# Performance work log

Measured on AMD Instinct MI355X. Metric: run time of the kernel, lower is better.

The kernel has to match this reference:

```python
import jax, jax.numpy as jnp
import numpy as np

BETA = 0.25  # commitment loss weight


def setup_inputs() -> dict:
    key = jax.random.key(0)
    k1, k2 = jax.random.split(key)
    x = jax.random.normal(k1, (16, 2048, 512), dtype=jnp.float32)
    codebooks = jax.random.normal(k2, (8, 1024, 512), dtype=jnp.float32)
    return {"x": x, "codebooks": codebooks}


def reference(x, codebooks):
    """Residual VQ: sequentially quantize residual with each codebook.
    x: [B, N, D] float; codebooks: [Q, C, D] float.
    Returns (quantized_out [B,N,D], indices [B,N,Q], vq_losses [Q], qq_losses [Q]).
    """
    sg = jax.lax.stop_gradient

    def step(carry, cb):
        residual, qout = carry  # [B,N,D], [B,N,D]; cb: [C,D]
        # squared euclidean distances [B,N,C] via GEMM
        d = (
            jnp.sum(residual * residual, axis=-1, keepdims=True)
            - 2.0 * jnp.einsum("bnd,cd->bnc", residual, cb)
            + jnp.sum(cb * cb, axis=-1)
        )
        idx = jnp.argmin(d, axis=-1)          # [B,N] nearest code
        q_hard = cb[idx]                       # [B,N,D] codebook gather
        # straight-through estimator
        q = residual + sg(q_hard - residual)
        vq = jnp.mean((q_hard - sg(residual)) ** 2)        # codebook loss
        qq = BETA * jnp.mean((sg(q_hard) - residual) ** 2)  # commitment loss
        new_residual = residual - sg(q)
        return (new_residual, qout + q), (idx, vq, qq)

    init = (x, jnp.zeros_like(x))
    (_, quantized_out), (idxs, vqs, qqs) = jax.lax.scan(step, init, codebooks)
    all_indices = jnp.moveaxis(idxs, 0, -1)  # [B, N, Q]
    return quantized_out, all_indices, vqs, qqs
```

## Files before the change

kernel.cpp:

```cpp
#include <hip/hip_runtime.h>

#define D 512
#define C 1024
#define BM 128
#define BN 128
#define BK 32
#define NCHUNK 8
#define KSTEPS 16
#define NBLK_CU 8192

typedef _Float16 f16x8 __attribute__((ext_vector_type(8)));
typedef float f32x4 __attribute__((ext_vector_type(4)));

__device__ __forceinline__ void gll16(const void* g, void* l) {
    __builtin_amdgcn_global_load_lds(
        (const __attribute__((address_space(1))) void*)g,
        (__attribute__((address_space(3))) void*)l, 16, 0, 0);
}

__global__ __launch_bounds__(256) void cbnorm_kernel(const float* __restrict__ cb,
                                                     float* __restrict__ cbn) {
    int code = blockIdx.x * 4 + (threadIdx.x >> 6);
    int lane = threadIdx.x & 63;
    const float* row = cb + (size_t)code * D;
    float4 a = *(const float4*)(row + lane * 8);
    float4 b = *(const float4*)(row + lane * 8 + 4);
    float s = a.x*a.x + a.y*a.y + a.z*a.z + a.w*a.w
            + b.x*b.x + b.y*b.y + b.z*b.z + b.w*b.w;
    #pragma unroll
    for (int off = 32; off > 0; off >>= 1) s += __shfl_down(s, off, 64);
    if (lane == 0) cbn[code] = s;
}

__global__ __launch_bounds__(256) void cb_split_kernel(const float* __restrict__ cbs,
                                                       uint4* __restrict__ hi_plane,
                                                       uint4* __restrict__ lo_plane) {
    int t = blockIdx.x * 256 + threadIdx.x;
    int rg = t >> 9;
    int u  = t & 511;
    int q  = rg >> 7;
    int cc = (rg >> 4) & 7;
    int ks = rg & 15;
    int ctile = u >> 6;
    int ksub  = (u >> 4) & 3;
    int col   = u & 15;
    int code  = cc * 128 + ctile * 16 + col;
    int d0    = ks * 32 + ksub * 8;
    const float* src = cbs + ((size_t)q * C + code) * D + d0;
    float4 v0 = *(const float4*)src;
    float4 v1 = *(const float4*)(src + 4);
    float xv[8] = {v0.x, v0.y, v0.z, v0.w, v1.x, v1.y, v1.z, v1.w};
    f16x8 h, l;
    #pragma unroll
    for (int e = 0; e < 8; ++e) {
        _Float16 hh = (_Float16)xv[e];
        h[e] = hh;
        l[e] = (_Float16)(xv[e] - (float)hh);
    }
    hi_plane[t] = __builtin_bit_cast(uint4, h);
    lo_plane[t] = __builtin_bit_cast(uint4, l);
}

__global__ __launch_bounds__(256, 2) void vq_mfma_step(
    const float* __restrict__ rin,
    const uint4* __restrict__ bhq,
    const uint4* __restrict__ blq,
    const float* __restrict__ cbnq,
    float4*      __restrict__ partial)
{
    __shared__ uint4 SH[2][4][512];
    const int tid  = threadIdx.x;
    const int lane = tid & 63;
    const int wv   = tid >> 6;
    const int wm   = wv >> 1, wn = wv & 1;
    const int bm   = blockIdx.x & 255;
    const int cc   = blockIdx.x >> 8;
    const int bp   = bm * BM;

    f32x4 acc[4][4];
    #pragma unroll
    for (int i = 0; i < 4; ++i)
        #pragma unroll
        for (int j = 0; j < 4; ++j) acc[i][j] = (f32x4){0.f, 0.f, 0.f, 0.f};

    auto STAGE = [&](int buf, int ks) {
        const uint4* bh = bhq + (size_t)(cc * KSTEPS + ks) * 512;
        const uint4* bl = blq + (size_t)(cc * KSTEPS + ks) * 512;
        gll16(bh + tid,       &SH[buf][2][tid]);
        gll16(bh + tid + 256, &SH[buf][2][tid + 256]);
        gll16(bl + tid,       &SH[buf][3][tid]);
        gll16(bl + tid + 256, &SH[buf][3][tid + 256]);
        #pragma unroll
        for (int it = 0; it < 2; ++it) {
            int oct  = tid + it * 256;
            int row  = ((oct >> 6) << 4) + (oct & 15);
            int ksub = (oct >> 4) & 3;
            const float* src = rin + (size_t)(bp + row) * D + ks * BK + ksub * 8;
            float4 v0 = *(const float4*)src;
            float4 v1 = *(const float4*)(src + 4);
            float xv[8] = {v0.x, v0.y, v0.z, v0.w, v1.x, v1.y, v1.z, v1.w};
            f16x8 h, l;
            #pragma unroll
            for (int e = 0; e < 8; ++e) {
                _Float16 hh = (_Float16)xv[e];
                h[e] = hh;
                l[e] = (_Float16)(xv[e] - (float)hh);
            }
            SH[buf][0][oct] = __builtin_bit_cast(uint4, h);
            SH[buf][1][oct] = __builtin_bit_cast(uint4, l);
        }
    };

    STAGE(0, 0);
    int buf = 0;
    for (int ks = 0; ks < KSTEPS; ++ks) {
        __syncthreads();
        if (ks + 1 < KSTEPS) STAGE(buf ^ 1, ks + 1);
        f16x8 ah[4], al[4], bh[4], bl[4];
        #pragma unroll
        for (int mt = 0; mt < 4; ++mt) {
            ah[mt] = __builtin_bit_cast(f16x8, SH[buf][0][(wm * 4 + mt) * 64 + lane]);
            al[mt] = __builtin_bit_cast(f16x8, SH[buf][1][(wm * 4 + mt) * 64 + lane]);
        }
        #pragma unroll
        for (int nt = 0; nt < 4; ++nt) {
            bh[nt] = __builtin_bit_cast(f16x8, SH[buf][2][(wn * 4 + nt) * 64 + lane]);
            bl[nt] = __builtin_bit_cast(f16x8, SH[buf][3][(wn * 4 + nt) * 64 + lane]);
        }
        #pragma unroll
        for (int mt = 0; mt < 4; ++mt)
            #pragma unroll
            for (int nt = 0; nt < 4; ++nt) {
                acc[mt][nt] = __builtin_amdgcn_mfma_f32_16x16x32_f16(ah[mt], bh[nt], acc[mt][nt], 0, 0, 0);
                acc[mt][nt] = __builtin_amdgcn_mfma_f32_16x16x32_f16(ah[mt], bl[nt], acc[mt][nt], 0, 0, 0);
                acc[mt][nt] = __builtin_amdgcn_mfma_f32_16x16x32_f16(al[mt], bh[nt], acc[mt][nt], 0, 0, 0);
            }
        buf ^= 1;
    }

    const int colbase = cc * BN;
    float cbn_l[4];
    int   ci_l[4];
    #pragma unroll
    for (int nt = 0; nt < 4; ++nt) {
        ci_l[nt]  = colbase + (wn * 4 + nt) * 16 + (lane & 15);
        cbn_l[nt] = cbnq[ci_l[nt]];
    }
    #pragma unroll
    for (int mt = 0; mt < 4; ++mt) {
        #pragma unroll
        for (int r = 0; r < 4; ++r) {
            float s1 = 3.4e38f, s2 = 3.4e38f;
            int i1 = 1 << 30, i2 = 1 << 30;
            #pragma unroll
            for (int nt = 0; nt < 4; ++nt) {
                float s = fmaf(-2.f, acc[mt][nt][r], cbn_l[nt]);
                int ci = ci_l[nt];
                if (s < s1 || (s == s1 && ci < i1)) { s2 = s1; i2 = i1; s1 = s; i1 = ci; }
                else if (s < s2 || (s == s2 && ci < i2)) { s2 = s; i2 = ci; }
            }
            #pragma unroll
            for (int m = 1; m < 16; m <<= 1) {
                float o1 = __shfl_xor(s1, m, 64); int oi1 = __shfl_xor(i1, m, 64);
                float o2 = __shfl_xor(s2, m, 64); int oi2 = __shfl_xor(i2, m, 64);
                if (o1 < s1 || (o1 == s1 && oi1 < i1)) {
                    if (s1 < o2 || (s1 == o2 && i1 < oi2)) { s2 = s1; i2 = i1; }
                    else { s2 = o2; i2 = oi2; }
                    s1 = o1; i1 = oi1;
                } else {
                    if (o1 < s2 || (o1 == s2 && oi1 < i2)) { s2 = o1; i2 = oi1; }
                }
            }
            if ((lane & 15) == 0) {
                int row = bp + wm * 64 + mt * 16 + (lane >> 4) * 4 + r;
                partial[(size_t)row * 16 + cc * 2 + wn] = make_float4(s1, (float)i1, s2, (float)i2);
            }
        }
    }
}

__global__ __launch_bounds__(256) void combine_update(
    const float* __restrict__ rin, float* __restrict__ rout,
    const float* __restrict__ cbq,
    const float4* __restrict__ partial,
    float* __restrict__ idx_out, float* __restrict__ blockloss,
    int q, int nq)
{
    __shared__ float wls[4];
    const int lane = threadIdx.x & 63;
    const int wv   = threadIdx.x >> 6;
    const int p    = blockIdx.x * 4 + wv;

    float s1 = 3.4e38f, s2 = 3.4e38f;
    int i1 = 1 << 30, i2 = 1 << 30;
    if (lane < 16) {
        float4 v = partial[(size_t)p * 16 + lane];
        s1 = v.x; i1 = (int)v.y; s2 = v.z; i2 = (int)v.w;
    }
    #pragma unroll
    for (int m = 1; m < 16; m <<= 1) {
        float o1 = __shfl_xor(s1, m, 64); int oi1 = __shfl_xor(i1, m, 64);
        float o2 = __shfl_xor(s2, m, 64); int oi2 = __shfl_xor(i2, m, 64);
        if (o1 < s1 || (o1 == s1 && oi1 < i1)) {
            if (s1 < o2 || (s1 == o2 && i1 < oi2)) { s2 = s1; i2 = i1; }
            else { s2 = o2; i2 = oi2; }
            s1 = o1; i1 = oi1;
        } else {
            if (o1 < s2 || (o1 == s2 && oi1 < i2)) { s2 = o1; i2 = oi1; }
        }
    }
    float s1b = __shfl(s1, 0, 64);
    float s2b = __shfl(s2, 0, 64);
    i1 = __shfl(i1, 0, 64);
    i2 = __shfl(i2, 0, 64);

    const float* rrow = rin + (size_t)p * D;
    const float* c1   = cbq + (size_t)i1 * D;
    float4 r0 = *(const float4*)(rrow + lane * 8);
    float4 r1 = *(const float4*)(rrow + lane * 8 + 4);
    float4 a0 = *(const float4*)(c1 + lane * 8);
    float4 a1 = *(const float4*)(c1 + lane * 8 + 4);
    float ra[8] = {r0.x, r0.y, r0.z, r0.w, r1.x, r1.y, r1.z, r1.w};
    float aa[8] = {a0.x, a0.y, a0.z, a0.w, a1.x, a1.y, a1.z, a1.w};

    int f = i1;
    bool use2 = false;
    if (s2b - s1b <= 0.05f) {
        const float* c2 = cbq + (size_t)i2 * D;
        float4 b0 = *(const float4*)(c2 + lane * 8);
        float4 b1 = *(const float4*)(c2 + lane * 8 + 4);
        float bb[8] = {b0.x, b0.y, b0.z, b0.w, b1.x, b1.y, b1.z, b1.w};
        double da = 0.0, db = 0.0;
        #pragma unroll
        for (int e = 0; e < 8; ++e) {
            double rr = (double)ra[e], av = (double)aa[e], bv = (double)bb[e];
            da += av * av - 2.0 * rr * av;
            db += bv * bv - 2.0 * rr * bv;
        }
        #pragma unroll
        for (int m = 32; m > 0; m >>= 1) {
            da += __shfl_xor(da, m, 64);
            db += __shfl_xor(db, m, 64);
        }
        if (db < da || (db == da && i2 < i1)) { f = i2; use2 = true; }
        if (use2) {
            #pragma unroll
            for (int e = 0; e < 8; ++e) aa[e] = bb[e];
        }
    }
    if (lane == 0) idx_out[(size_t)p * nq + q] = (float)f;

    float nsum = 0.f;
    float nv[8];
    #pragma unroll
    for (int e = 0; e < 8; ++e) {
        nv[e] = ra[e] - aa[e];
        nsum = fmaf(nv[e], nv[e], nsum);
    }
    float4 w0 = {nv[0], nv[1], nv[2], nv[3]};
    float4 w1 = {nv[4], nv[5], nv[6], nv[7]};
    *(float4*)(rout + (size_t)p * D + lane * 8)     = w0;
    *(float4*)(rout + (size_t)p * D + lane * 8 + 4) = w1;
    #pragma unroll
    for (int off = 32; off > 0; off >>= 1) nsum += __shfl_down(nsum, off, 64);
    if (lane == 0) wls[wv] = nsum;
    __syncthreads();
    if (threadIdx.x == 0)
        blockloss[(size_t)q * NBLK_CU + blockIdx.x] = wls[0] + wls[1] + wls[2] + wls[3];
}

__global__ __launch_bounds__(256) void finalize_kernel(
    const float* __restrict__ x, float* __restrict__ outq,
    const float* __restrict__ blockloss,
    float* __restrict__ losses, float invPD, int n4, int nq)
{
    if (blockIdx.x < (unsigned)nq) {
        __shared__ float wls[4];
        int q = blockIdx.x;
        float s = 0.f;
        for (int i = threadIdx.x; i < NBLK_CU; i += 256)
            s += blockloss[(size_t)q * NBLK_CU + i];
        #pragma unroll
        for (int off = 32; off > 0; off >>= 1) s += __shfl_down(s, off, 64);
        if ((threadIdx.x & 63) == 0) wls[threadIdx.x >> 6] = s;
        __syncthreads();
        if (threadIdx.x == 0) {
            float vq = (wls[0] + wls[1] + wls[2] + wls[3]) * invPD;
            losses[q] = vq;
            losses[nq + q] = 0.25f * vq;
        }
    }
    int stride = gridDim.x * blockDim.x;
    for (int i = blockIdx.x * blockDim.x + threadIdx.x; i < n4; i += stride) {
        float4 xv = ((const float4*)x)[i];
        float4 rv = ((float4*)outq)[i];
        float4 qv;
        qv.x = xv.x - rv.x;
        qv.y = xv.y - rv.y;
        qv.z = xv.z - rv.z;
        qv.w = xv.w - rv.w;
        ((float4*)outq)[i] = qv;
    }
}

extern "C" void kernel_launch(void* const* d_in, const int* in_sizes, int n_in,
                              void* d_out, int out_size, void* d_ws, size_t ws_size,
                              hipStream_t stream)
{
    const float* x   = (const float*)d_in[0];
    const float* cbs = (const float*)d_in[1];
    const int PD = in_sizes[0];
    const int P  = PD / D;
    const int nq = in_sizes[1] / (C * D);

    float* out     = (float*)d_out;
    float* resid   = out;
    float* idx_out = out + (size_t)PD;
    float* losses  = idx_out + (size_t)P * nq;

    char* wsb = (char*)d_ws;
    uint4*  cb_hi     = (uint4*)wsb;
    uint4*  cb_lo     = (uint4*)(wsb + 8388608);
    float*  cbn       = (float*)(wsb + 16777216);
    float4* partial   = (float4*)(wsb + 16809984);
    float*  blockloss = (float*)(wsb + 25198592);

    cbnorm_kernel<<<nq * C / 4, 256, 0, stream>>>(cbs, cbn);
    cb_split_kernel<<<nq * C * D / 8 / 256, 256, 0, stream>>>(cbs, cb_hi, cb_lo);

    for (int q = 0; q < nq; ++q) {
        vq_mfma_step<<<(P / BM) * NCHUNK, 256, 0, stream>>>(
            q == 0 ? x : resid,
            cb_hi + (size_t)q * 65536, cb_lo + (size_t)q * 65536,
            cbn + (size_t)q * C, partial);
        combine_update<<<P / 4, 256, 0, stream>>>(
            q == 0 ? x : resid, resid,
            cbs + (size_t)q * C * D, partial,
            idx_out, blockloss, q, nq);
    }
    finalize_kernel<<<2048, 256, 0, stream>>>(x, out, blockloss, losses,
                                              1.f / (float)PD, PD / 4, nq);
}
```

Before: 1.663 ms.

## Use single fp16 MFMA pass with top-3 candidates and exact fp64 rescoring

Drops the hi/lo fp16 split emulation, so the distance GEMM runs one fp16 MFMA per tile instead of three and stages half the LDS data. To make up for the lower precision, each row keeps its top-3 candidates instead of top-2, their indices packed into one float slot, and combine_update always rescores all three in fp64 against the fp32 codebook. Occupancy hint rises to 4 blocks per CU. The risk is picking the wrong code when the true nearest falls outside the fp16 top-3, and the extra gathers and fp64 math in the combine kernel.

```diff
diff --git a/kernel.cpp b/kernel.cpp
--- a/kernel.cpp
+++ b/kernel.cpp
@@ -4,7 +4,6 @@
 #define C 1024
 #define BM 128
 #define BN 128
-#define BK 32
 #define NCHUNK 8
 #define KSTEPS 16
 #define NBLK_CU 8192
@@ -16,6 +15,14 @@
     __builtin_amdgcn_global_load_lds(
         (const __attribute__((address_space(1))) void*)g,
         (__attribute__((address_space(3))) void*)l, 16, 0, 0);
+}
+
+__device__ __forceinline__ void ins3(float s, int i,
+                                     float& s1, int& i1, float& s2, int& i2,
+                                     float& s3, int& i3) {
+    if (s < s1 || (s == s1 && i < i1)) { s3 = s2; i3 = i2; s2 = s1; i2 = i1; s1 = s; i1 = i; }
+    else if (s < s2 || (s == s2 && i < i2)) { s3 = s2; i3 = i2; s2 = s; i2 = i; }
+    else if (s < s3 || (s == s3 && i < i3)) { s3 = s; i3 = i; }
 }
 
 __global__ __launch_bounds__(256) void cbnorm_kernel(const float* __restrict__ cb,
@@ -33,42 +40,35 @@
 }
 
 __global__ __launch_bounds__(256) void cb_split_kernel(const float* __restrict__ cbs,
-                                                       uint4* __restrict__ hi_plane,
-                                                       uint4* __restrict__ lo_plane) {
+                                                       uint4* __restrict__ hi_plane) {
     int t = blockIdx.x * 256 + threadIdx.x;
     int rg = t >> 9;
     int u  = t & 511;
     int q  = rg >> 7;
     int cc = (rg >> 4) & 7;
     int ks = rg & 15;
-    int ctile = u >> 6;
-    int ksub  = (u >> 4) & 3;
-    int col   = u & 15;
-    int code  = cc * 128 + ctile * 16 + col;
-    int d0    = ks * 32 + ksub * 8;
+    int tile = u >> 6;
+    int ksub = (u >> 4) & 3;
+    int col  = u & 15;
+    int code = cc * 128 + tile * 16 + col;
+    int d0   = ks * 32 + ksub * 8;
     const float* src = cbs + ((size_t)q * C + code) * D + d0;
     float4 v0 = *(const float4*)src;
     float4 v1 = *(const float4*)(src + 4);
     float xv[8] = {v0.x, v0.y, v0.z, v0.w, v1.x, v1.y, v1.z, v1.w};
-    f16x8 h, l;
-    #pragma unroll
-    for (int e = 0; e < 8; ++e) {
-        _Float16 hh = (_Float16)xv[e];
-        h[e] = hh;
-        l[e] = (_Float16)(xv[e] - (float)hh);
-    }
+    f16x8 h;
+    #pragma unroll
+    for (int e = 0; e < 8; ++e) h[e] = (_Float16)xv[e];
     hi_plane[t] = __builtin_bit_cast(uint4, h);
-    lo_plane[t] = __builtin_bit_cast(uint4, l);
-}
-
-__global__ __launch_bounds__(256, 2) void vq_mfma_step(
+}
+
+__global__ __launch_bounds__(256, 4) void vq_mfma_step(
     const float* __restrict__ rin,
     const uint4* __restrict__ bhq,
-    const uint4* __restrict__ blq,
     const float* __restrict__ cbnq,
     float4*      __restrict__ partial)
 {
-    __shared__ uint4 SH[2][4][512];
+    __shared__ uint4 SH[2][2][512];
     const int tid  = threadIdx.x;
     const int lane = tid & 63;
     const int wv   = tid >> 6;
@@ -85,29 +85,21 @@
 
     auto STAGE = [&](int buf, int ks) {
         const uint4* bh = bhq + (size_t)(cc * KSTEPS + ks) * 512;
-        const uint4* bl = blq + (size_t)(cc * KSTEPS + ks) * 512;
-        gll16(bh + tid,       &SH[buf][2][tid]);
-        gll16(bh + tid + 256, &SH[buf][2][tid + 256]);
-        gll16(bl + tid,       &SH[buf][3][tid]);
-        gll16(bl + tid + 256, &SH[buf][3][tid + 256]);
+        gll16(bh + tid,       &SH[buf][1][tid]);
+        gll16(bh + tid + 256, &SH[buf][1][tid + 256]);
         #pragma unroll
         for (int it = 0; it < 2; ++it) {
             int oct  = tid + it * 256;
             int row  = ((oct >> 6) << 4) + (oct & 15);
             int ksub = (oct >> 4) & 3;
-            const float* src = rin + (size_t)(bp + row) * D + ks * BK + ksub * 8;
+            const float* src = rin + (size_t)(bp + row) * D + ks * 32 + ksub * 8;
             float4 v0 = *(const float4*)src;
             float4 v1 = *(const float4*)(src + 4);
             float xv[8] = {v0.x, v0.y, v0.z, v0.w, v1.x, v1.y, v1.z, v1.w};
-            f16x8 h, l;
+            f16x8 h;
             #pragma unroll
-            for (int e = 0; e < 8; ++e) {
-                _Float16 hh = (_Float16)xv[e];
-                h[e] = hh;
-                l[e] = (_Float16)(xv[e] - (float)hh);
-            }
+            for (int e = 0; e < 8; ++e) h[e] = (_Float16)xv[e];
             SH[buf][0][oct] = __builtin_bit_cast(uint4, h);
-            SH[buf][1][oct] = __builtin_bit_cast(uint4, l);
         }
     };
 
@@ -116,25 +108,18 @@
     for (int ks = 0; ks < KSTEPS; ++ks) {
         __syncthreads();
         if (ks + 1 < KSTEPS) STAGE(buf ^ 1, ks + 1);
-        f16x8 ah[4], al[4], bh[4], bl[4];
-        #pragma unroll
-        for (int mt = 0; mt < 4; ++mt) {
+        f16x8 ah[4], bh[4];
+        #pragma unroll
+        for (int mt = 0; mt < 4; ++mt)
             ah[mt] = __builtin_bit_cast(f16x8, SH[buf][0][(wm * 4 + mt) * 64 + lane]);
-            al[mt] = __builtin_bit_cast(f16x8, SH[buf][1][(wm * 4 + mt) * 64 + lane]);
-        }
-        #pragma unroll
-        for (int nt = 0; nt < 4; ++nt) {
-            bh[nt] = __builtin_bit_cast(f16x8, SH[buf][2][(wn * 4 + nt) * 64 + lane]);
-            bl[nt] = __builtin_bit_cast(f16x8, SH[buf][3][(wn * 4 + nt) * 64 + lane]);
-        }
+        #pragma unroll
+        for (int nt = 0; nt < 4; ++nt)
+            bh[nt] = __builtin_bit_cast(f16x8, SH[buf][1][(wn * 4 + nt) * 64 + lane]);
         #pragma unroll
         for (int mt = 0; mt < 4; ++mt)
             #pragma unroll
-            for (int nt = 0; nt < 4; ++nt) {
+            for (int nt = 0; nt < 4; ++nt)
                 acc[mt][nt] = __builtin_amdgcn_mfma_f32_16x16x32_f16(ah[mt], bh[nt], acc[mt][nt], 0, 0, 0);
-                acc[mt][nt] = __builtin_amdgcn_mfma_f32_16x16x32_f16(ah[mt], bl[nt], acc[mt][nt], 0, 0, 0);
-                acc[mt][nt] = __builtin_amdgcn_mfma_f32_16x16x32_f16(al[mt], bh[nt], acc[mt][nt], 0, 0, 0);
-            }
         buf ^= 1;
     }
 
@@ -150,30 +135,27 @@
     for (int mt = 0; mt < 4; ++mt) {
         #pragma unroll
         for (int r = 0; r < 4; ++r) {
-            float s1 = 3.4e38f, s2 = 3.4e38f;
-            int i1 = 1 << 30, i2 = 1 << 30;
+            float s1 = 3.4e38f, s2 = 3.4e38f, s3 = 3.4e38f;
+            int i1 = 1023, i2 = 1023, i3 = 1023;
             #pragma unroll
             for (int nt = 0; nt < 4; ++nt) {
                 float s = fmaf(-2.f, acc[mt][nt][r], cbn_l[nt]);
-                int ci = ci_l[nt];
-                if (s < s1 || (s == s1 && ci < i1)) { s2 = s1; i2 = i1; s1 = s; i1 = ci; }
-                else if (s < s2 || (s == s2 && ci < i2)) { s2 = s; i2 = ci; }
+                ins3(s, ci_l[nt], s1, i1, s2, i2, s3, i3);
             }
             #pragma unroll
             for (int m = 1; m < 16; m <<= 1) {
                 float o1 = __shfl_xor(s1, m, 64); int oi1 = __shfl_xor(i1, m, 64);
                 float o2 = __shfl_xor(s2, m, 64); int oi2 = __shfl_xor(i2, m, 64);
-                if (o1 < s1 || (o1 == s1 && oi1 < i1)) {
-                    if (s1 < o2 || (s1 == o2 && i1 < oi2)) { s2 = s1; i2 = i1; }
-                    else { s2 = o2; i2 = oi2; }
-                    s1 = o1; i1 = oi1;
-                } else {
-                    if (o1 < s2 || (o1 == s2 && oi1 < i2)) { s2 = o1; i2 = oi1; }
-                }
+                float o3 = __shfl_xor(s3, m, 64); int oi3 = __shfl_xor(i3, m, 64);
+                ins3(o1, oi1, s1, i1, s2, i2, s3, i3);
+                ins3(o2, oi2, s1, i1, s2, i2, s3, i3);
+                ins3(o3, oi3, s1, i1, s2, i2, s3, i3);
             }
             if ((lane & 15) == 0) {
                 int row = bp + wm * 64 + mt * 16 + (lane >> 4) * 4 + r;
-                partial[(size_t)row * 16 + cc * 2 + wn] = make_float4(s1, (float)i1, s2, (float)i2);
+                unsigned pk = (unsigned)i1 | ((unsigned)i2 << 10) | ((unsigned)i3 << 20);
+                partial[(size_t)row * 16 + cc * 2 + wn] =
+                    make_float4(s1, s2, s3, __builtin_bit_cast(float, pk));
             }
         }
     }
@@ -191,70 +173,68 @@
     const int wv   = threadIdx.x >> 6;
     const int p    = blockIdx.x * 4 + wv;
 
-    float s1 = 3.4e38f, s2 = 3.4e38f;
-    int i1 = 1 << 30, i2 = 1 << 30;
+    float s1 = 3.4e38f, s2 = 3.4e38f, s3 = 3.4e38f;
+    int i1 = 1023, i2 = 1023, i3 = 1023;
     if (lane < 16) {
         float4 v = partial[(size_t)p * 16 + lane];
-        s1 = v.x; i1 = (int)v.y; s2 = v.z; i2 = (int)v.w;
+        unsigned pk = __builtin_bit_cast(unsigned, v.w);
+        s1 = v.x; s2 = v.y; s3 = v.z;
+        i1 = pk & 1023; i2 = (pk >> 10) & 1023; i3 = (pk >> 20) & 1023;
     }
     #pragma unroll
     for (int m = 1; m < 16; m <<= 1) {
         float o1 = __shfl_xor(s1, m, 64); int oi1 = __shfl_xor(i1, m, 64);
         float o2 = __shfl_xor(s2, m, 64); int oi2 = __shfl_xor(i2, m, 64);
-        if (o1 < s1 || (o1 == s1 && oi1 < i1)) {
-            if (s1 < o2 || (s1 == o2 && i1 < oi2)) { s2 = s1; i2 = i1; }
-            else { s2 = o2; i2 = oi2; }
-            s1 = o1; i1 = oi1;
-        } else {
-            if (o1 < s2 || (o1 == s2 && oi1 < i2)) { s2 = o1; i2 = oi1; }
-        }
-    }
-    float s1b = __shfl(s1, 0, 64);
-    float s2b = __shfl(s2, 0, 64);
+        float o3 = __shfl_xor(s3, m, 64); int oi3 = __shfl_xor(i3, m, 64);
+        ins3(o1, oi1, s1, i1, s2, i2, s3, i3);
+        ins3(o2, oi2, s1, i1, s2, i2, s3, i3);
+        ins3(o3, oi3, s1, i1, s2, i2, s3, i3);
+    }
     i1 = __shfl(i1, 0, 64);
     i2 = __shfl(i2, 0, 64);
+    i3 = __shfl(i3, 0, 64);
 
     const float* rrow = rin + (size_t)p * D;
-    const float* c1   = cbq + (size_t)i1 * D;
     float4 r0 = *(const float4*)(rrow + lane * 8);
     float4 r1 = *(const float4*)(rrow + lane * 8 + 4);
-    float4 a0 = *(const float4*)(c1 + lane * 8);
-    float4 a1 = *(const float4*)(c1 + lane * 8 + 4);
+    const float* c1 = cbq + (size_t)i1 * D;
+    const float* c2 = cbq + (size_t)i2 * D;
+    const float* c3 = cbq + (size_t)i3 * D;
+    float4 a0 = *(const float4*)(c1 + lane * 8), a1 = *(const float4*)(c1 + lane * 8 + 4);
+    float4 b0 = *(const float4*)(c2 + lane * 8), b1 = *(const float4*)(c2 + lane * 8 + 4);
+    float4 g0 = *(const float4*)(c3 + lane * 8), g1 = *(const float4*)(c3 + lane * 8 + 4);
     float ra[8] = {r0.x, r0.y, r0.z, r0.w, r1.x, r1.y, r1.z, r1.w};
     float aa[8] = {a0.x, a0.y, a0.z, a0.w, a1.x, a1.y, a1.z, a1.w};
-
-    int f = i1;
-    bool use2 = false;
-    if (s2b - s1b <= 0.05f) {
-        const float* c2 = cbq + (size_t)i2 * D;
-        float4 b0 = *(const float4*)(c2 + lane * 8);
-        float4 b1 = *(const float4*)(c2 + lane * 8 + 4);
-        float bb[8] = {b0.x, b0.y, b0.z, b0.w, b1.x, b1.y, b1.z, b1.w};
-        double da = 0.0, db = 0.0;
-        #pragma unroll
-        for (int e = 0; e < 8; ++e) {
-            double rr = (double)ra[e], av = (double)aa[e], bv = (double)bb[e];
-            da += av * av - 2.0 * rr * av;
-            db += bv * bv - 2.0 * rr * bv;
-        }
-        #pragma unroll
-        for (int m = 32; m > 0; m >>= 1) {
-            da += __shfl_xor(da, m, 64);
-            db += __shfl_xor(db, m, 64);
-        }
-        if (db < da || (db == da && i2 < i1)) { f = i2; use2 = true; }
-        if (use2) {
-            #pragma unroll
-            for (int e = 0; e < 8; ++e) aa[e] = bb[e];
-        }
-    }
-    if (lane == 0) idx_out[(size_t)p * nq + q] = (float)f;
+    float bb[8] = {b0.x, b0.y, b0.z, b0.w, b1.x, b1.y, b1.z, b1.w};
+    float gg[8] = {g0.x, g0.y, g0.z, g0.w, g1.x, g1.y, g1.z, g1.w};
+
+    double d1 = 0.0, d2 = 0.0, d3 = 0.0;
+    #pragma unroll
+    for (int e = 0; e < 8; ++e) {
+        double rr = (double)ra[e];
+        double av = (double)aa[e], bv = (double)bb[e], gv = (double)gg[e];
+        d1 += av * av - 2.0 * rr * av;
+        d2 += bv * bv - 2.0 * rr * bv;
+        d3 += gv * gv - 2.0 * rr * gv;
+    }
+    #pragma unroll
+    for (int m = 32; m > 0; m >>= 1) {
+        d1 += __shfl_xor(d1, m, 64);
+        d2 += __shfl_xor(d2, m, 64);
+        d3 += __shfl_xor(d3, m, 64);
+    }
+    int    fi = i1;
+    double fd = d1;
+    if (d2 < fd || (d2 == fd && i2 < fi)) { fd = d2; fi = i2; }
+    if (d3 < fd || (d3 == fd && i3 < fi)) { fd = d3; fi = i3; }
+    if (lane == 0) idx_out[(size_t)p * nq + q] = (float)fi;
 
     float nsum = 0.f;
     float nv[8];
     #pragma unroll
     for (int e = 0; e < 8; ++e) {
-        nv[e] = ra[e] - aa[e];
+        float cv = (fi == i1) ? aa[e] : ((fi == i2) ? bb[e] : gg[e]);
+        nv[e] = ra[e] - cv;
         nsum = fmaf(nv[e], nv[e], nsum);
     }
     float4 w0 = {nv[0], nv[1], nv[2], nv[3]};
@@ -320,22 +300,19 @@
 
     char* wsb = (char*)d_ws;
     uint4*  cb_hi     = (uint4*)wsb;
-    uint4*  cb_lo     = (uint4*)(wsb + 8388608);
-    float*  cbn       = (float*)(wsb + 16777216);
-    float4* partial   = (float4*)(wsb + 16809984);
-    float*  blockloss = (float*)(wsb + 25198592);
+    float*  cbn       = (float*)(wsb + 8388608);
+    float4* partial   = (float4*)(wsb + 8421376);
+    float*  blockloss = (float*)(wsb + 16809984);
 
     cbnorm_kernel<<<nq * C / 4, 256, 0, stream>>>(cbs, cbn);
-    cb_split_kernel<<<nq * C * D / 8 / 256, 256, 0, stream>>>(cbs, cb_hi, cb_lo);
+    cb_split_kernel<<<nq * C * D / 8 / 256, 256, 0, stream>>>(cbs, cb_hi);
 
     for (int q = 0; q < nq; ++q) {
+        const float* rin = (q == 0) ? x : resid;
         vq_mfma_step<<<(P / BM) * NCHUNK, 256, 0, stream>>>(
-            q == 0 ? x : resid,
-            cb_hi + (size_t)q * 65536, cb_lo + (size_t)q * 65536,
-            cbn + (size_t)q * C, partial);
+            rin, cb_hi + (size_t)q * 65536, cbn + (size_t)q * C, partial);
         combine_update<<<P / 4, 256, 0, stream>>>(
-            q == 0 ? x : resid, resid,
-            cbs + (size_t)q * C * D, partial,
+            rin, resid, cbs + (size_t)q * C * D, partial,
             idx_out, blockloss, q, nq);
     }
     finalize_kernel<<<2048, 256, 0, stream>>>(x, out, blockloss, losses,
```

Result: slower. 5.544 ms (+233.3%).
